# Performance work log

Measured on AMD Instinct MI355X. Metric: run time of the kernel, lower is better.

## Reference

```python
import jax, jax.numpy as jnp
import numpy as np

N_NODES = 100000
N_EDGES = 1600000
IN_DIM = 128
OUT_DIM = 128


def setup_inputs() -> dict:
    key = jax.random.key(0)
    k1, k2, k3, k4 = jax.random.split(key, 4)
    x = jax.random.normal(k1, (N_NODES, IN_DIM), dtype=jnp.float32)
    edge_index = jax.random.randint(k2, (2, N_EDGES), 0, N_NODES, dtype=jnp.int64)
    # glorot-ish linear weight, bias, and PReLU per-channel slope (torch default 0.25)
    W = jax.random.normal(k3, (IN_DIM, OUT_DIM), dtype=jnp.float32) * (1.0 / np.sqrt(IN_DIM))
    b = jax.random.normal(k4, (OUT_DIM,), dtype=jnp.float32) * 0.01
    alpha = jnp.full((OUT_DIM,), 0.25, dtype=jnp.float32)
    return {"x": x, "edge_index": edge_index, "W": W, "b": b, "alpha": alpha}


def reference(x, edge_index, W, b, alpha):
    N = x.shape[0]
    # add self loops (GCNConv default add_self_loops=True)
    loop = jnp.arange(N, dtype=edge_index.dtype)
    src = jnp.concatenate([edge_index[0], loop])  # [E+N]
    dst = jnp.concatenate([edge_index[1], loop])
    # symmetric normalization: deg computed at targets (includes self loops)
    ones = jnp.ones(dst.shape[0], dtype=x.dtype)
    deg = jax.ops.segment_sum(ones, dst, num_segments=N)  # [N]
    dinv = jnp.where(deg > 0, jax.lax.rsqrt(deg), 0.0)
    norm = dinv[src] * dinv[dst]  # [E+N]
    # dense linear transform, then gather-normalize-scatter aggregation
    h = x @ W  # [N, OUT_DIM]
    msg = h[src] * norm[:, None]  # [E+N, OUT_DIM]
    agg = jax.ops.segment_sum(msg, dst, num_segments=N) + b  # [N, OUT_DIM]
    # PReLU with per-channel slope
    z = jnp.where(agg > 0, agg, alpha * agg)
    return z
```

## Files before the change

kernel.cpp:

```cpp
#include <hip/hip_runtime.h>
#include <hip/hip_bf16.h>
#include <cstdint>

#define DIM 128
#define BK_SHIFT 7
#define BK_NODES 128
#define MAX_BUCKETS 1024
#define CUR_STRIDE 16
#define ST 4096
#define EPT 16
#define CAP 2560

typedef float f32x4  __attribute__((ext_vector_type(4)));
typedef short bf16x8 __attribute__((ext_vector_type(8)));

__device__ __forceinline__ unsigned bf16_rne(float f) {
    unsigned u = __float_as_uint(f);
    return (u + 0x7fffu + ((u >> 16) & 1u)) >> 16;
}

__global__ __launch_bounds__(256) void init_kernel(const float* __restrict__ x,
                                                   ushort* __restrict__ y,
                                                   const float* __restrict__ W,
                                                   ushort* __restrict__ Wt,
                                                   int* __restrict__ bcursor,
                                                   int N, int pb, int wb, int nbk) {
    int b = blockIdx.x, tid = threadIdx.x;
    if (b < pb) {
        int t = b * 256 + tid;
        if (t < N * (DIM / 4)) {
            float4 v = ((const float4*)x)[t];
            uint2 o;
            o.x = bf16_rne(v.x) | (bf16_rne(v.y) << 16);
            o.y = bf16_rne(v.z) | (bf16_rne(v.w) << 16);
            ((uint2*)y)[t] = o;
        }
    } else if (b < pb + wb) {
        int idx = (b - pb) * 256 + tid;
        if (idx < DIM * DIM) {
            int k = idx >> 7, c = idx & (DIM - 1);
            Wt[c * DIM + k] = (ushort)bf16_rne(W[idx]);
        }
    } else {
        int idx = (b - pb - wb) * 256 + tid;
        if (idx < nbk * CUR_STRIDE) bcursor[idx] = 0;
    }
}

__global__ __launch_bounds__(256) void scatter_kernel(const int* __restrict__ src,
                                                      const int* __restrict__ dst,
                                                      int* __restrict__ bcursor,
                                                      int* __restrict__ bbuf,
                                                      int E, int nbk) {
    __shared__ int h[MAX_BUCKETS];
    for (int i = threadIdx.x; i < nbk; i += 256) h[i] = 0;
    __syncthreads();
    int base = blockIdx.x * ST;
    int bk[EPT], rk[EPT], pk[EPT];
    #pragma unroll
    for (int k = 0; k < EPT; ++k) {
        int e = base + k * 256 + threadIdx.x;
        bk[k] = -1;
        if (e < E) {
            int d = dst[e];
            int b = ((unsigned)d) >> BK_SHIFT;
            bk[k] = b;
            pk[k] = (src[e] << BK_SHIFT) | (d & (BK_NODES - 1));
            rk[k] = atomicAdd(&h[b], 1);
        }
    }
    __syncthreads();
    for (int i = threadIdx.x; i < nbk; i += 256) {
        int c = h[i];
        h[i] = c ? atomicAdd(&bcursor[i * CUR_STRIDE], c) : 0;
    }
    __syncthreads();
    #pragma unroll
    for (int k = 0; k < EPT; ++k) {
        if (bk[k] >= 0) {
            int pos = h[bk[k]] + rk[k];
            if (pos < CAP) bbuf[(size_t)bk[k] * CAP + pos] = pk[k];
        }
    }
}

__global__ __launch_bounds__(256) void build_csr_kernel(const int* __restrict__ bbuf,
                                                        const int* __restrict__ bcursor,
                                                        int* __restrict__ obeg,
                                                        int* __restrict__ oend,
                                                        float* __restrict__ dinv,
                                                        int* __restrict__ csr_src,
                                                        int N) {
    __shared__ int cnt[BK_NODES];
    __shared__ int sc[BK_NODES];
    __shared__ int cur[BK_NODES];
    int b = blockIdx.x, tid = threadIdx.x;
    int count = bcursor[b * CUR_STRIDE];
    if (count > CAP) count = CAP;
    int base = b * CAP;
    if (tid < BK_NODES) cnt[tid] = 0;
    __syncthreads();
    for (int j = tid; j < count; j += 256)
        atomicAdd(&cnt[bbuf[base + j] & (BK_NODES - 1)], 1);
    __syncthreads();
    if (tid < BK_NODES) sc[tid] = cnt[tid];
    __syncthreads();
    for (int d = 1; d < BK_NODES; d <<= 1) {
        int v = (tid >= d && tid < BK_NODES) ? sc[tid - d] : 0;
        __syncthreads();
        if (tid < BK_NODES) sc[tid] += v;
        __syncthreads();
    }
    if (tid < BK_NODES) {
        int node = b * BK_NODES + tid;
        int start = base + sc[tid] - cnt[tid];
        cur[tid] = start;
        if (node < N) {
            obeg[node] = start;
            oend[node] = start + cnt[tid];
            dinv[node] = rsqrtf((float)(cnt[tid] + 1));
        }
    }
    __syncthreads();
    for (int j = tid; j < count; j += 256) {
        int p = bbuf[base + j];
        int pos = atomicAdd(&cur[p & (BK_NODES - 1)], 1);
        csr_src[pos] = p >> BK_SHIFT;
    }
}

__global__ __launch_bounds__(256) void agg_kernel(const ushort* __restrict__ y,
                                                  const int* __restrict__ csr_src,
                                                  const int* __restrict__ obeg,
                                                  const int* __restrict__ oend,
                                                  const float* __restrict__ dinv,
                                                  ushort* __restrict__ h, int N) {
    int lane = threadIdx.x & 63;
    int wid  = __builtin_amdgcn_readfirstlane((int)(threadIdx.x >> 6));
    int node = blockIdx.x * 4 + wid;
    if (node >= N) return;
    int beg = obeg[node];
    int end = oend[node];
    float di = dinv[node];
    unsigned v = ((const unsigned*)(y + (size_t)node * DIM))[lane];
    float ax = di * __uint_as_float(v << 16);
    float ay = di * __uint_as_float(v & 0xffff0000u);
    int j = beg;
    for (; j + 4 <= end; j += 4) {
        int s0 = csr_src[j + 0], s1 = csr_src[j + 1];
        int s2 = csr_src[j + 2], s3 = csr_src[j + 3];
        float w0 = dinv[s0], w1 = dinv[s1], w2 = dinv[s2], w3 = dinv[s3];
        unsigned v0 = ((const unsigned*)(y + (size_t)s0 * DIM))[lane];
        unsigned v1 = ((const unsigned*)(y + (size_t)s1 * DIM))[lane];
        unsigned v2 = ((const unsigned*)(y + (size_t)s2 * DIM))[lane];
        unsigned v3 = ((const unsigned*)(y + (size_t)s3 * DIM))[lane];
        ax += w0 * __uint_as_float(v0 << 16); ay += w0 * __uint_as_float(v0 & 0xffff0000u);
        ax += w1 * __uint_as_float(v1 << 16); ay += w1 * __uint_as_float(v1 & 0xffff0000u);
        ax += w2 * __uint_as_float(v2 << 16); ay += w2 * __uint_as_float(v2 & 0xffff0000u);
        ax += w3 * __uint_as_float(v3 << 16); ay += w3 * __uint_as_float(v3 & 0xffff0000u);
    }
    for (; j < end; ++j) {
        int s = csr_src[j];
        float w = dinv[s];
        unsigned vv = ((const unsigned*)(y + (size_t)s * DIM))[lane];
        ax += w * __uint_as_float(vv << 16); ay += w * __uint_as_float(vv & 0xffff0000u);
    }
    ax *= di; ay *= di;
    ((unsigned*)(h + (size_t)node * DIM))[lane] = bf16_rne(ax) | (bf16_rne(ay) << 16);
}

__global__ __launch_bounds__(256) void gemm_kernel(const ushort* __restrict__ h,
                                                   const ushort* __restrict__ Wt,
                                                   const float* __restrict__ bias,
                                                   const float* __restrict__ alpha,
                                                   float* __restrict__ out, int N) {
    int lane = threadIdx.x & 63;
    int wv   = threadIdx.x >> 6;
    int rowbase = (blockIdx.x * 4 + wv) * 16;
    int r = lane & 15, quad = lane >> 4;
    f32x4 acc[8];
    #pragma unroll
    for (int ct = 0; ct < 8; ++ct) acc[ct] = (f32x4){0.f, 0.f, 0.f, 0.f};
    int arow = rowbase + r;
    if (arow >= N) arow = N - 1;
    const ushort* ap = h + (size_t)arow * DIM + quad * 8;
    #pragma unroll
    for (int ks = 0; ks < 4; ++ks) {
        bf16x8 a = *(const bf16x8*)(ap + ks * 32);
        #pragma unroll
        for (int ct = 0; ct < 8; ++ct) {
            bf16x8 b = *(const bf16x8*)(Wt + (size_t)(ct * 16 + r) * DIM + ks * 32 + quad * 8);
            acc[ct] = __builtin_amdgcn_mfma_f32_16x16x32_bf16(a, b, acc[ct], 0, 0, 0);
        }
    }
    #pragma unroll
    for (int ct = 0; ct < 8; ++ct) {
        int col = ct * 16 + r;
        float bb = bias[col], al = alpha[col];
        #pragma unroll
        for (int reg = 0; reg < 4; ++reg) {
            int grow = rowbase + quad * 4 + reg;
            if (grow < N) {
                float vv = acc[ct][reg] + bb;
                vv = vv > 0.f ? vv : al * vv;
                out[(size_t)grow * DIM + col] = vv;
            }
        }
    }
}

extern "C" void kernel_launch(void* const* d_in, const int* in_sizes, int n_in,
                              void* d_out, int out_size, void* d_ws, size_t ws_size,
                              hipStream_t stream) {
    const float* x     = (const float*)d_in[0];
    const int*   ei    = (const int*)d_in[1];
    const float* W     = (const float*)d_in[2];
    const float* bias  = (const float*)d_in[3];
    const float* alpha = (const float*)d_in[4];
    float* out = (float*)d_out;

    int N = in_sizes[0] / DIM;
    int E = in_sizes[1] / 2;
    const int* src = ei;
    const int* dst = ei + E;
    int nbk = (N + BK_NODES - 1) >> BK_SHIFT;

    char* ws = (char*)d_ws;
    size_t off = 0;
    auto alloc = [&](size_t bytes) -> char* {
        char* p = ws + off;
        off += (bytes + 255) & ~(size_t)255;
        return p;
    };
    size_t h_bytes    = (size_t)N * DIM * 2;
    size_t bbuf_bytes = (size_t)nbk * CAP * 4;
    char*   hreg    = alloc(h_bytes > bbuf_bytes ? h_bytes : bbuf_bytes);
    ushort* h       = (ushort*)hreg;
    int*    bbuf    = (int*)hreg;
    int*    csr_src = (int*)alloc((size_t)nbk * CAP * 4);
    ushort* y       = (ushort*)alloc((size_t)N * DIM * 2);
    int*    bcursor = (int*)alloc((size_t)nbk * CUR_STRIDE * 4);
    int*    obeg    = (int*)alloc((size_t)N * 4);
    int*    oend    = (int*)alloc((size_t)N * 4);
    float*  dinv    = (float*)alloc((size_t)N * 4);
    ushort* Wt      = (ushort*)alloc((size_t)DIM * DIM * 2);

    int pb = (N * (DIM / 4) + 255) / 256;
    int wb = (DIM * DIM + 255) / 256;
    int zb = (nbk * CUR_STRIDE + 255) / 256;

    init_kernel<<<pb + wb + zb, 256, 0, stream>>>(x, y, W, Wt, bcursor, N, pb, wb, nbk);
    scatter_kernel<<<(E + ST - 1) / ST, 256, 0, stream>>>(src, dst, bcursor, bbuf, E, nbk);
    build_csr_kernel<<<nbk, 256, 0, stream>>>(bbuf, bcursor, obeg, oend, dinv, csr_src, N);
    agg_kernel<<<(N + 3) / 4, 256, 0, stream>>>(y, csr_src, obeg, oend, dinv, h, N);
    gemm_kernel<<<(N + 63) / 64, 256, 0, stream>>>(h, Wt, bias, alpha, out, N);
}
```

Before: 262.5 us.

## Split wavefront into four edge groups with 16-byte row loads in aggregation

The aggregation kernel now divides each 64-lane wavefront into four 16-lane groups. Each group loads a full 256-byte bf16 row with uint4 loads and handles a different edge, so a wave keeps eight edges in flight per iteration instead of four serial 4-byte-per-lane loads. Partial sums are combined with cross-group shuffles and only group 0 writes the result. This aims to raise memory-level parallelism in the gather. It adds shuffle overhead, wastes lanes on clamped padding edges for low-degree nodes, and raises register use for the eight accumulators.

Result: no change. 262.5 us (-0.0%).

```diff
diff --git a/kernel.cpp b/kernel.cpp
--- a/kernel.cpp
+++ b/kernel.cpp
@@ -129,6 +129,17 @@
     }
 }
 
+__device__ __forceinline__ void agg_accum(float* a, uint4 v, float wt) {
+    a[0] += wt * __uint_as_float(v.x << 16);
+    a[1] += wt * __uint_as_float(v.x & 0xffff0000u);
+    a[2] += wt * __uint_as_float(v.y << 16);
+    a[3] += wt * __uint_as_float(v.y & 0xffff0000u);
+    a[4] += wt * __uint_as_float(v.z << 16);
+    a[5] += wt * __uint_as_float(v.z & 0xffff0000u);
+    a[6] += wt * __uint_as_float(v.w << 16);
+    a[7] += wt * __uint_as_float(v.w & 0xffff0000u);
+}
+
 __global__ __launch_bounds__(256) void agg_kernel(const ushort* __restrict__ y,
                                                   const int* __restrict__ csr_src,
                                                   const int* __restrict__ obeg,
@@ -139,34 +150,50 @@
     int wid  = __builtin_amdgcn_readfirstlane((int)(threadIdx.x >> 6));
     int node = blockIdx.x * 4 + wid;
     if (node >= N) return;
+    int g = lane >> 4;
+    int m = lane & 15;
     int beg = obeg[node];
-    int end = oend[node];
+    int cnt = oend[node] - beg;
     float di = dinv[node];
-    unsigned v = ((const unsigned*)(y + (size_t)node * DIM))[lane];
-    float ax = di * __uint_as_float(v << 16);
-    float ay = di * __uint_as_float(v & 0xffff0000u);
-    int j = beg;
-    for (; j + 4 <= end; j += 4) {
-        int s0 = csr_src[j + 0], s1 = csr_src[j + 1];
-        int s2 = csr_src[j + 2], s3 = csr_src[j + 3];
-        float w0 = dinv[s0], w1 = dinv[s1], w2 = dinv[s2], w3 = dinv[s3];
-        unsigned v0 = ((const unsigned*)(y + (size_t)s0 * DIM))[lane];
-        unsigned v1 = ((const unsigned*)(y + (size_t)s1 * DIM))[lane];
-        unsigned v2 = ((const unsigned*)(y + (size_t)s2 * DIM))[lane];
-        unsigned v3 = ((const unsigned*)(y + (size_t)s3 * DIM))[lane];
-        ax += w0 * __uint_as_float(v0 << 16); ay += w0 * __uint_as_float(v0 & 0xffff0000u);
-        ax += w1 * __uint_as_float(v1 << 16); ay += w1 * __uint_as_float(v1 & 0xffff0000u);
-        ax += w2 * __uint_as_float(v2 << 16); ay += w2 * __uint_as_float(v2 & 0xffff0000u);
-        ax += w3 * __uint_as_float(v3 << 16); ay += w3 * __uint_as_float(v3 & 0xffff0000u);
-    }
-    for (; j < end; ++j) {
-        int s = csr_src[j];
-        float w = dinv[s];
-        unsigned vv = ((const unsigned*)(y + (size_t)s * DIM))[lane];
-        ax += w * __uint_as_float(vv << 16); ay += w * __uint_as_float(vv & 0xffff0000u);
-    }
-    ax *= di; ay *= di;
-    ((unsigned*)(h + (size_t)node * DIM))[lane] = bf16_rne(ax) | (bf16_rne(ay) << 16);
+    float a[8];
+    #pragma unroll
+    for (int c = 0; c < 8; ++c) a[c] = 0.f;
+
+    {
+        uint4 v = ((const uint4*)(y + (size_t)node * DIM))[m];
+        agg_accum(a, v, (g == 0) ? di : 0.f);
+    }
+
+    int t = g;
+    int nit = (cnt + 7) >> 3;
+    for (int it = 0; it < nit; ++it, t += 8) {
+        int tB = t + 4;
+        int iA = beg + (t  < cnt ? t  : cnt - 1);
+        int iB = beg + (tB < cnt ? tB : cnt - 1);
+        int sA = csr_src[iA];
+        int sB = csr_src[iB];
+        float wA = (t  < cnt) ? dinv[sA] : 0.f;
+        float wB = (tB < cnt) ? dinv[sB] : 0.f;
+        uint4 vA = ((const uint4*)(y + (size_t)sA * DIM))[m];
+        uint4 vB = ((const uint4*)(y + (size_t)sB * DIM))[m];
+        agg_accum(a, vA, wA);
+        agg_accum(a, vB, wB);
+    }
+
+    #pragma unroll
+    for (int c = 0; c < 8; ++c) {
+        a[c] += __shfl_xor(a[c], 16);
+        a[c] += __shfl_xor(a[c], 32);
+    }
+
+    if (g == 0) {
+        uint4 o;
+        o.x = bf16_rne(di * a[0]) | (bf16_rne(di * a[1]) << 16);
+        o.y = bf16_rne(di * a[2]) | (bf16_rne(di * a[3]) << 16);
+        o.z = bf16_rne(di * a[4]) | (bf16_rne(di * a[5]) << 16);
+        o.w = bf16_rne(di * a[6]) | (bf16_rne(di * a[7]) << 16);
+        ((uint4*)(h + (size_t)node * DIM))[m] = o;
+    }
 }
 
 __global__ __launch_bounds__(256) void gemm_kernel(const ushort* __restrict__ h,
```
